# Performance work log

Hardware: AMD Instinct MI355X
Metric: run time of the kernel (lower is better)

## Reference

```python
import jax, jax.numpy as jnp
import numpy as np

N = 4096      # nodes
IN = 512      # in_features
H = 8         # heads
D = 64        # out_features // heads (out % heads == 0)
EDGE_PROB = 0.01


def setup_inputs() -> dict:
    key = jax.random.key(0)
    kx, ka, kw, ko, kd = jax.random.split(key, 5)
    x = jax.random.normal(kx, (N, IN), dtype=jnp.float32)
    # dense binary adjacency with self-loops (original indexes adj[loc, :] as a mask)
    adj = (jax.random.uniform(ka, (N, N)) < EDGE_PROB).astype(jnp.float32)
    adj = jnp.maximum(adj, jnp.eye(N, dtype=jnp.float32))
    # stacked per-head params (original keeps Python lists of equal-sized heads)
    W = jax.random.normal(kw, (H, IN, D), dtype=jnp.float32) * (1.0 / np.sqrt(IN))
    a_origin = jax.random.normal(ko, (H, D), dtype=jnp.float32) * 0.1
    a_dst = jax.random.normal(kd, (H, D), dtype=jnp.float32) * 0.1
    return {"x": x, "adj": adj, "W": W, "a_origin": a_origin, "a_dst": a_dst}


def reference(x, adj, W, a_origin, a_dst):
    # per-head projection: mx[h] = x @ W[h]  -> [H, N, D]
    mx = jnp.einsum('nf,hfd->hnd', x, W)
    # clacAttn: e_ij = exp(mx_i . a_origin + mx_j . a_dst), masked by adj[i,:], row-normalised
    s_i = jnp.einsum('hnd,hd->hn', mx, a_origin)   # source term (row)
    t_j = jnp.einsum('hnd,hd->hn', mx, a_dst)      # dest term (col)
    logits = s_i[:, :, None] + t_j[:, None, :]     # [H, N, N]
    neg_inf = jnp.finfo(logits.dtype).min
    masked = jnp.where(adj[None] > 0, logits, neg_inf)
    attn = jax.nn.softmax(masked, axis=-1)         # == exp/masked-sum of original
    out_h = jnp.einsum('hij,hjd->hid', attn, mx)   # [H, N, D]
    # hstack over heads -> [N, H*D]
    return jnp.transpose(out_h, (1, 0, 2)).reshape(N, H * D)
```

## Files before the change

### kernel.cpp

```cpp
#include <hip/hip_runtime.h>
#include <hip/hip_bf16.h>

#define N_NODES 4096
#define IN_F    512
#define HEADS   8
#define DH      64
#define HD      512

typedef __bf16 bf16x8 __attribute__((ext_vector_type(8)));
typedef float  f32x4  __attribute__((ext_vector_type(4)));

__device__ __forceinline__ float bf_lo(unsigned u) { return __uint_as_float(u << 16); }
__device__ __forceinline__ float bf_hi(unsigned u) { return __uint_as_float(u & 0xffff0000u); }

#define KP 72

__global__ __launch_bounds__(256, 2) void k1_gemm(const float* __restrict__ X,
                                                  const float* __restrict__ W,
                                                  const float* __restrict__ a_dst,
                                                  __bf16* __restrict__ C,
                                                  float* __restrict__ et) {
    __shared__ __bf16 As[2][64][KP];
    __shared__ __bf16 Bs[2][64][KP];
    __shared__ float  ts[2][64];
    int tid  = threadIdx.x;
    int h    = blockIdx.x & 7;
    int y    = blockIdx.x >> 3;
    int row0 = y * 64, col0 = h * 64;
    int wave = tid >> 6, lane = tid & 63;
    int wm = wave >> 1, wn = wave & 1;
    int lr = lane & 15, kg = lane >> 4;

    f32x4 acc[2][2] = {};

    int sr = tid >> 3, sc = (tid & 7) * 8;
    const float* aptr0 = X + (size_t)(row0 + sr) * IN_F + sc;
    const float* aptr1 = aptr0 + (size_t)32 * IN_F;
    int dcol = tid & 63, fq = (tid >> 6) * 16;
    const float* wptr = W + ((size_t)h * IN_F + fq) * DH + dcol;

    f32x4 pa00 = *(const f32x4*)aptr0, pa01 = *(const f32x4*)(aptr0 + 4);
    f32x4 pa10 = *(const f32x4*)aptr1, pa11 = *(const f32x4*)(aptr1 + 4);
    float wv[16];
    #pragma unroll
    for (int i = 0; i < 16; ++i) wv[i] = wptr[(size_t)i * DH];

    float ad0 = a_dst[h * DH + wn * 32 + lr];
    float ad1 = a_dst[h * DH + wn * 32 + 16 + lr];

    #pragma unroll
    for (int k = 0; k < IN_F / 64; ++k) {
        int cur = k & 1;
        bf16x8 a0 = { (__bf16)pa00[0], (__bf16)pa00[1], (__bf16)pa00[2], (__bf16)pa00[3],
                      (__bf16)pa01[0], (__bf16)pa01[1], (__bf16)pa01[2], (__bf16)pa01[3] };
        bf16x8 a1 = { (__bf16)pa10[0], (__bf16)pa10[1], (__bf16)pa10[2], (__bf16)pa10[3],
                      (__bf16)pa11[0], (__bf16)pa11[1], (__bf16)pa11[2], (__bf16)pa11[3] };
        bf16x8 b0 = { (__bf16)wv[0],  (__bf16)wv[1],  (__bf16)wv[2],  (__bf16)wv[3],
                      (__bf16)wv[4],  (__bf16)wv[5],  (__bf16)wv[6],  (__bf16)wv[7] };
        bf16x8 b1 = { (__bf16)wv[8],  (__bf16)wv[9],  (__bf16)wv[10], (__bf16)wv[11],
                      (__bf16)wv[12], (__bf16)wv[13], (__bf16)wv[14], (__bf16)wv[15] };
        *(bf16x8*)&As[cur][sr][sc]        = a0;
        *(bf16x8*)&As[cur][sr + 32][sc]   = a1;
        *(bf16x8*)&Bs[cur][dcol][fq]      = b0;
        *(bf16x8*)&Bs[cur][dcol][fq + 8]  = b1;
        if (k + 1 < IN_F / 64) {
            int off = (k + 1) * 64;
            pa00 = *(const f32x4*)(aptr0 + off); pa01 = *(const f32x4*)(aptr0 + off + 4);
            pa10 = *(const f32x4*)(aptr1 + off); pa11 = *(const f32x4*)(aptr1 + off + 4);
            const float* wp = wptr + (size_t)off * DH;
            #pragma unroll
            for (int i = 0; i < 16; ++i) wv[i] = wp[(size_t)i * DH];
        }
        __syncthreads();
        #pragma unroll
        for (int kc = 0; kc < 2; ++kc) {
            bf16x8 af0 = *(const bf16x8*)&As[cur][wm * 32 + lr]     [kc * 32 + kg * 8];
            bf16x8 af1 = *(const bf16x8*)&As[cur][wm * 32 + 16 + lr][kc * 32 + kg * 8];
            bf16x8 bf0 = *(const bf16x8*)&Bs[cur][wn * 32 + lr]     [kc * 32 + kg * 8];
            bf16x8 bf1 = *(const bf16x8*)&Bs[cur][wn * 32 + 16 + lr][kc * 32 + kg * 8];
            acc[0][0] = __builtin_amdgcn_mfma_f32_16x16x32_bf16(af0, bf0, acc[0][0], 0, 0, 0);
            acc[0][1] = __builtin_amdgcn_mfma_f32_16x16x32_bf16(af0, bf1, acc[0][1], 0, 0, 0);
            acc[1][0] = __builtin_amdgcn_mfma_f32_16x16x32_bf16(af1, bf0, acc[1][0], 0, 0, 0);
            acc[1][1] = __builtin_amdgcn_mfma_f32_16x16x32_bf16(af1, bf1, acc[1][1], 0, 0, 0);
        }
    }

    #pragma unroll
    for (int mt = 0; mt < 2; ++mt) {
        #pragma unroll
        for (int nt = 0; nt < 2; ++nt) {
            int col = col0 + wn * 32 + nt * 16 + lr;
            #pragma unroll
            for (int r = 0; r < 4; ++r) {
                int row = row0 + wm * 32 + mt * 16 + kg * 4 + r;
                C[(size_t)row * HD + col] = (__bf16)acc[mt][nt][r];
            }
        }
    }
    #pragma unroll
    for (int mt = 0; mt < 2; ++mt) {
        #pragma unroll
        for (int r = 0; r < 4; ++r) {
            float p = ad0 * acc[mt][0][r] + ad1 * acc[mt][1][r];
            p += __shfl_xor(p, 1);
            p += __shfl_xor(p, 2);
            p += __shfl_xor(p, 4);
            p += __shfl_xor(p, 8);
            if (lr == 0) ts[wn][wm * 32 + mt * 16 + kg * 4 + r] = p;
        }
    }
    __syncthreads();
    if (tid < 64) {
        float t = ts[0][tid] + ts[1][tid];
        et[(size_t)(row0 + tid) * HEADS + h] = __expf(t);
    }
}

#define MAXNBR 512
__global__ __launch_bounds__(256) void k3_aggr(const float* __restrict__ adj,
                                               const __bf16* __restrict__ mx,
                                               const float* __restrict__ et,
                                               float* __restrict__ out) {
    __shared__ int   jlist[MAXNBR];
    __shared__ float el[MAXNBR * 8];
    __shared__ int   cnt;
    int tid = threadIdx.x;
    int i   = blockIdx.x;
    if (tid == 0) cnt = 0;
    __syncthreads();

    {
        const float* arow = adj + (size_t)i * N_NODES;
        int j0 = tid * 16;
        #pragma unroll
        for (int q = 0; q < 4; ++q) {
            uint4 p = *(const uint4*)(arow + j0 + q * 4);
            int jb = j0 + q * 4;
            if (p.x) { int s = atomicAdd(&cnt, 1); if (s < MAXNBR) jlist[s] = jb;     }
            if (p.y) { int s = atomicAdd(&cnt, 1); if (s < MAXNBR) jlist[s] = jb + 1; }
            if (p.z) { int s = atomicAdd(&cnt, 1); if (s < MAXNBR) jlist[s] = jb + 2; }
            if (p.w) { int s = atomicAdd(&cnt, 1); if (s < MAXNBR) jlist[s] = jb + 3; }
        }
    }
    __syncthreads();
    int c = cnt < MAXNBR ? cnt : MAXNBR;

    for (int idx = tid; idx < c * 8; idx += 256)
        el[idx] = et[(size_t)jlist[idx >> 3] * 8 + (idx & 7)];
    __syncthreads();

    int h = tid >> 5;
    const unsigned* mxu = (const unsigned*)mx;
    float a0 = 0.f, a1 = 0.f, d = 0.f;
    int k = 0;
    for (; k + 4 <= c; k += 4) {
        int j0_ = jlist[k], j1_ = jlist[k+1], j2_ = jlist[k+2], j3_ = jlist[k+3];
        float e0 = el[(k    ) * 8 + h], e1 = el[(k + 1) * 8 + h];
        float e2 = el[(k + 2) * 8 + h], e3 = el[(k + 3) * 8 + h];
        unsigned p0 = mxu[(size_t)j0_ * 256 + tid];
        unsigned p1 = mxu[(size_t)j1_ * 256 + tid];
        unsigned p2 = mxu[(size_t)j2_ * 256 + tid];
        unsigned p3 = mxu[(size_t)j3_ * 256 + tid];
        a0 += e0 * bf_lo(p0) + e1 * bf_lo(p1) + e2 * bf_lo(p2) + e3 * bf_lo(p3);
        a1 += e0 * bf_hi(p0) + e1 * bf_hi(p1) + e2 * bf_hi(p2) + e3 * bf_hi(p3);
        d  += e0 + e1 + e2 + e3;
    }
    for (; k < c; ++k) {
        int j = jlist[k];
        float e = el[k * 8 + h];
        unsigned p = mxu[(size_t)j * 256 + tid];
        a0 += e * bf_lo(p);
        a1 += e * bf_hi(p);
        d  += e;
    }
    float inv = 1.f / d;
    out[(size_t)i * HD + tid * 2]     = a0 * inv;
    out[(size_t)i * HD + tid * 2 + 1] = a1 * inv;
}

extern "C" void kernel_launch(void* const* d_in, const int* in_sizes, int n_in,
                              void* d_out, int out_size, void* d_ws, size_t ws_size,
                              hipStream_t stream) {
    const float* x     = (const float*)d_in[0];
    const float* adj   = (const float*)d_in[1];
    const float* W     = (const float*)d_in[2];
    const float* a_dst = (const float*)d_in[4];
    float* out = (float*)d_out;

    char* ws = (char*)d_ws;
    __bf16* mx = (__bf16*)ws;
    float*  et = (float*)(ws + 4194304);

    k1_gemm<<<dim3(512), dim3(256), 0, stream>>>(x, W, a_dst, mx, et);
    k3_aggr<<<dim3(N_NODES), dim3(256), 0, stream>>>(adj, mx, et, out);
}
```

Measured before the change: 134.3 us.

## Restructure aggregation: wave-scan neighbor compaction, per-wave neighbor split, 16B gathers

```diff
diff --git a/kernel.cpp b/kernel.cpp
--- a/kernel.cpp
+++ b/kernel.cpp
@@ -122,60 +122,113 @@
                                                const float* __restrict__ et,
                                                float* __restrict__ out) {
     __shared__ int   jlist[MAXNBR];
-    __shared__ float el[MAXNBR * 8];
     __shared__ int   cnt;
-    int tid = threadIdx.x;
-    int i   = blockIdx.x;
+    __shared__ float red[3][64][9];
+    int tid  = threadIdx.x;
+    int i    = blockIdx.x;
+    int w    = tid >> 6, lane = tid & 63;
     if (tid == 0) cnt = 0;
-    __syncthreads();
-
-    {
-        const float* arow = adj + (size_t)i * N_NODES;
-        int j0 = tid * 16;
-        #pragma unroll
-        for (int q = 0; q < 4; ++q) {
-            uint4 p = *(const uint4*)(arow + j0 + q * 4);
-            int jb = j0 + q * 4;
-            if (p.x) { int s = atomicAdd(&cnt, 1); if (s < MAXNBR) jlist[s] = jb;     }
-            if (p.y) { int s = atomicAdd(&cnt, 1); if (s < MAXNBR) jlist[s] = jb + 1; }
-            if (p.z) { int s = atomicAdd(&cnt, 1); if (s < MAXNBR) jlist[s] = jb + 2; }
-            if (p.w) { int s = atomicAdd(&cnt, 1); if (s < MAXNBR) jlist[s] = jb + 3; }
-        }
-    }
-    __syncthreads();
-    int c = cnt < MAXNBR ? cnt : MAXNBR;
-
-    for (int idx = tid; idx < c * 8; idx += 256)
-        el[idx] = et[(size_t)jlist[idx >> 3] * 8 + (idx & 7)];
-    __syncthreads();
-
-    int h = tid >> 5;
-    const unsigned* mxu = (const unsigned*)mx;
-    float a0 = 0.f, a1 = 0.f, d = 0.f;
-    int k = 0;
-    for (; k + 4 <= c; k += 4) {
-        int j0_ = jlist[k], j1_ = jlist[k+1], j2_ = jlist[k+2], j3_ = jlist[k+3];
-        float e0 = el[(k    ) * 8 + h], e1 = el[(k + 1) * 8 + h];
-        float e2 = el[(k + 2) * 8 + h], e3 = el[(k + 3) * 8 + h];
-        unsigned p0 = mxu[(size_t)j0_ * 256 + tid];
-        unsigned p1 = mxu[(size_t)j1_ * 256 + tid];
-        unsigned p2 = mxu[(size_t)j2_ * 256 + tid];
-        unsigned p3 = mxu[(size_t)j3_ * 256 + tid];
-        a0 += e0 * bf_lo(p0) + e1 * bf_lo(p1) + e2 * bf_lo(p2) + e3 * bf_lo(p3);
-        a1 += e0 * bf_hi(p0) + e1 * bf_hi(p1) + e2 * bf_hi(p2) + e3 * bf_hi(p3);
-        d  += e0 + e1 + e2 + e3;
-    }
-    for (; k < c; ++k) {
-        int j = jlist[k];
-        float e = el[k * 8 + h];
-        unsigned p = mxu[(size_t)j * 256 + tid];
-        a0 += e * bf_lo(p);
-        a1 += e * bf_hi(p);
-        d  += e;
-    }
-    float inv = 1.f / d;
-    out[(size_t)i * HD + tid * 2]     = a0 * inv;
-    out[(size_t)i * HD + tid * 2 + 1] = a1 * inv;
+
+    const uint4* arow = (const uint4*)(adj + (size_t)i * N_NODES);
+    uint4 v0 = arow[tid];
+    uint4 v1 = arow[256 + tid];
+    uint4 v2 = arow[512 + tid];
+    uint4 v3 = arow[768 + tid];
+    int n = (v0.x != 0) + (v0.y != 0) + (v0.z != 0) + (v0.w != 0)
+          + (v1.x != 0) + (v1.y != 0) + (v1.z != 0) + (v1.w != 0)
+          + (v2.x != 0) + (v2.y != 0) + (v2.z != 0) + (v2.w != 0)
+          + (v3.x != 0) + (v3.y != 0) + (v3.z != 0) + (v3.w != 0);
+    __syncthreads();
+
+    int pre = n;
+    #pragma unroll
+    for (int dlt = 1; dlt < 64; dlt <<= 1) {
+        int t = __shfl_up(pre, dlt, 64);
+        if (lane >= dlt) pre += t;
+    }
+    int wtot = __shfl(pre, 63, 64);
+    int base = 0;
+    if (lane == 63) base = atomicAdd(&cnt, wtot);
+    base = __shfl(base, 63, 64);
+    if (base + wtot <= MAXNBR) {
+        int p_ = base + pre - n;
+        int jb = tid * 4;
+        if (v0.x) jlist[p_++] = jb;
+        if (v0.y) jlist[p_++] = jb + 1;
+        if (v0.z) jlist[p_++] = jb + 2;
+        if (v0.w) jlist[p_++] = jb + 3;
+        jb += 1024;
+        if (v1.x) jlist[p_++] = jb;
+        if (v1.y) jlist[p_++] = jb + 1;
+        if (v1.z) jlist[p_++] = jb + 2;
+        if (v1.w) jlist[p_++] = jb + 3;
+        jb += 1024;
+        if (v2.x) jlist[p_++] = jb;
+        if (v2.y) jlist[p_++] = jb + 1;
+        if (v2.z) jlist[p_++] = jb + 2;
+        if (v2.w) jlist[p_++] = jb + 3;
+        jb += 1024;
+        if (v3.x) jlist[p_++] = jb;
+        if (v3.y) jlist[p_++] = jb + 1;
+        if (v3.z) jlist[p_++] = jb + 2;
+        if (v3.w) jlist[p_++] = jb + 3;
+    }
+    __syncthreads();
+    int c = cnt;
+    if (c > MAXNBR) c = MAXNBR;
+
+    int h = lane >> 3;
+    const uint4* mxv = (const uint4*)mx;
+    float acc[8] = {0.f, 0.f, 0.f, 0.f, 0.f, 0.f, 0.f, 0.f};
+    float d = 0.f;
+
+    int  k    = w;
+    bool more = (k < c);
+    int  j    = more ? jlist[k] : 0;
+    float e   = 0.f;
+    uint4 p   = {0u, 0u, 0u, 0u};
+    if (more) {
+        e = et[j * HEADS + h];
+        p = mxv[(size_t)j * 64 + lane];
+    }
+    while (more) {
+        int  k2   = k + 4;
+        bool m2   = (k2 < c);
+        int  j2   = m2 ? jlist[k2] : 0;
+        float e2  = 0.f;
+        uint4 p2  = {0u, 0u, 0u, 0u};
+        if (m2) {
+            e2 = et[j2 * HEADS + h];
+            p2 = mxv[(size_t)j2 * 64 + lane];
+        }
+        acc[0] += e * bf_lo(p.x);  acc[1] += e * bf_hi(p.x);
+        acc[2] += e * bf_lo(p.y);  acc[3] += e * bf_hi(p.y);
+        acc[4] += e * bf_lo(p.z);  acc[5] += e * bf_hi(p.z);
+        acc[6] += e * bf_lo(p.w);  acc[7] += e * bf_hi(p.w);
+        d += e;
+        k = k2; more = m2; j = j2; e = e2; p = p2;
+    }
+
+    if (w > 0) {
+        #pragma unroll
+        for (int q = 0; q < 8; ++q) red[w - 1][lane][q] = acc[q];
+        red[w - 1][lane][8] = d;
+    }
+    __syncthreads();
+    if (w == 0) {
+        #pragma unroll
+        for (int g = 0; g < 3; ++g) {
+            #pragma unroll
+            for (int q = 0; q < 8; ++q) acc[q] += red[g][lane][q];
+            d += red[g][lane][8];
+        }
+        float inv = 1.f / d;
+        f32x4 o0 = { acc[0] * inv, acc[1] * inv, acc[2] * inv, acc[3] * inv };
+        f32x4 o1 = { acc[4] * inv, acc[5] * inv, acc[6] * inv, acc[7] * inv };
+        float* orow = out + (size_t)i * HD + lane * 8;
+        *(f32x4*)orow       = o0;
+        *(f32x4*)(orow + 4) = o1;
+    }
 }
 
 extern "C" void kernel_launch(void* const* d_in, const int* in_sizes, int n_in,
```

After: 127.9 us. -4.8%, faster.
